# Kernel tuning notes

Hardware: AMD Instinct MI355X
Metric: run time of the kernel (lower is better)

## Reference

```python
import jax, jax.numpy as jnp
import numpy as np


def setup_inputs() -> dict:
    key = jax.random.key(0)
    k0, k1, k2, k3, k4, k5 = jax.random.split(key, 6)
    B, V, Fin, K, Fout = 8, 49152, 64, 3, 64
    nnz = V * 8  # ~8 neighbors per vertex (HEALPix sphere graph)
    std = (2.0 / (Fin * K)) ** 0.5  # Kaiming-normal as in reset_parameters
    inputs = jax.random.normal(k0, (B, V, Fin), jnp.float32)
    weight = jax.random.normal(k1, (Fin, K, Fout), jnp.float32) * std
    bias = jax.random.normal(k2, (Fout,), jnp.float32) * 0.05
    lap_rows = jax.random.randint(k3, (nnz,), 0, V, jnp.int32)
    lap_cols = jax.random.randint(k4, (nnz,), 0, V, jnp.int32)
    lap_vals = jax.random.normal(k5, (nnz,), jnp.float32) * 0.1
    return {"inputs": inputs, "weight": weight, "bias": bias,
            "lap_rows": lap_rows, "lap_cols": lap_cols, "lap_vals": lap_vals}


def reference(inputs, weight, bias, lap_rows, lap_cols, lap_vals):
    B, V, Fin = inputs.shape
    _, K, Fout = weight.shape

    def spmm(x):  # sparse Laplacian (COO) @ dense [V, Fin*B]
        return jax.ops.segment_sum(lap_vals[:, None] * x[lap_cols], lap_rows,
                                   num_segments=V)

    # x0: [V, Fin*B], matching torch's permute(1,2,0).view(V, Fin*B)
    x0 = inputs.transpose(1, 2, 0).reshape(V, Fin * B)
    xs = [x0]
    if K > 1:
        x1 = spmm(x0)
        xs.append(x1)
    for _ in range(2, K):
        x2 = 2.0 * spmm(x1) - x0  # Chebyshev recurrence
        xs.append(x2)
        x0, x1 = x1, x2
    x = jnp.stack(xs)                                    # [K, V, Fin*B]
    x = x.reshape(K, V, Fin, B).transpose(3, 1, 2, 0)    # [B, V, Fin, K]
    x = x.reshape(B * V, Fin * K)
    out = x @ weight.reshape(Fin * K, Fout)              # dense GEMM
    return out.reshape(B, V, Fout) + bias
```

## Files before the change

kernel.cpp:

```cpp
#include <hip/hip_runtime.h>
#include <hip/hip_bf16.h>
#include <stdint.h>

#define B_   8
#define V_   49152
#define M_   (B_ * V_)
#define GEMM_BLOCKS 1536

typedef unsigned short ushort_t;
typedef __attribute__((ext_vector_type(8))) short short8;
typedef __attribute__((ext_vector_type(4))) float float4v;

__device__ __forceinline__ float bf2f_lo(unsigned int pk) {
    union { unsigned int u; float f; } x; x.u = pk << 16; return x.f;
}
__device__ __forceinline__ float bf2f_hi(unsigned int pk) {
    union { unsigned int u; float f; } x; x.u = pk & 0xffff0000u; return x.f;
}
__device__ __forceinline__ ushort_t f2bf(float f) {
    union { unsigned int u; float f; } x; x.f = f;
    unsigned int u = x.u;
    unsigned int r = u + 0x7fffu + ((u >> 16) & 1u);
    return (ushort_t)(r >> 16);
}
__device__ __forceinline__ unsigned int pack2(float a, float b) {
    return ((unsigned int)f2bf(b) << 16) | (unsigned int)f2bf(a);
}

__global__ void fill_sentinel(float* out, int n) {
    int i = blockIdx.x * blockDim.x + threadIdx.x;
    if (i < n) out[i] = 9999.0f;
}

__global__ void zero_kernel(int* p, int n) {
    int i = blockIdx.x * blockDim.x + threadIdx.x;
    if (i < n) p[i] = 0;
}

__global__ void hist_kernel(const int* __restrict__ rows, int nnz, int* __restrict__ counts) {
    int i = blockIdx.x * blockDim.x + threadIdx.x;
    if (i < nnz) atomicAdd(&counts[rows[i]], 1);
}

__global__ __launch_bounds__(1024) void scan_kernel(const int* __restrict__ counts,
                                                    int* __restrict__ offsets) {
    __shared__ int s[1024];
    int t = threadIdx.x;
    const int C = V_ / 1024;
    int base_i = t * C;
    int sum = 0;
    for (int j = 0; j < C; j++) sum += counts[base_i + j];
    s[t] = sum;
    __syncthreads();
    for (int off = 1; off < 1024; off <<= 1) {
        int v = (t >= off) ? s[t - off] : 0;
        __syncthreads();
        s[t] += v;
        __syncthreads();
    }
    int run = (t == 0) ? 0 : s[t - 1];
    for (int j = 0; j < C; j++) {
        offsets[base_i + j] = run;
        run += counts[base_i + j];
    }
    if (t == 1023) offsets[V_] = run;
}

__global__ void bucket_kernel(const int* __restrict__ rows, const int* __restrict__ cols,
                              const float* __restrict__ vals, int nnz,
                              const int* __restrict__ offsets, int* __restrict__ cursor,
                              int* __restrict__ e_col, float* __restrict__ e_val) {
    int i = blockIdx.x * blockDim.x + threadIdx.x;
    if (i >= nnz) return;
    int r = rows[i];
    int p = offsets[r] + atomicAdd(&cursor[r], 1);
    e_col[p] = cols[i];
    e_val[p] = vals[i];
}

__global__ __launch_bounds__(256) void prep_x0t(const float* __restrict__ inp,
                                                ushort_t* __restrict__ x0t) {
    int idx = blockIdx.x * 256 + threadIdx.x;
    int f2 = idx & 31, v = idx >> 5;
    #pragma unroll
    for (int b = 0; b < 8; b++) {
        const float* src = inp + ((size_t)b * V_ + v) * 64 + f2 * 2;
        float2 d = *(const float2*)src;
        *(unsigned int*)(x0t + ((size_t)v * 8 + b) * 64 + f2 * 2) = pack2(d.x, d.y);
    }
}

__global__ void prep_w(const float* __restrict__ wgt, ushort_t* __restrict__ wBf) {
    int idx = blockIdx.x * 256 + threadIdx.x;
    if (idx >= 6 * 4 * 64 * 8) return;
    int j = idx & 7, lane = (idx >> 3) & 63, nt = (idx >> 9) & 3, kb = idx >> 11;
    int k = kb * 32 + (lane >> 4) * 8 + j;
    int kc = k >> 6, fi = k & 63;
    int fo = nt * 16 + (lane & 15);
    wBf[idx] = f2bf(wgt[(fi * 3 + kc) * 64 + fo]);
}

__global__ __launch_bounds__(256) void spmm1_kernel(const ushort_t* __restrict__ x0t,
                                                    const int* __restrict__ offsets,
                                                    const int* __restrict__ e_col,
                                                    const float* __restrict__ e_val,
                                                    ushort_t* __restrict__ x1) {
    int v = blockIdx.x, tid = threadIdx.x;
    int b = tid >> 5, f2 = tid & 31;
    int base = b * 64 + f2 * 2;
    __shared__ int   s_col[64];
    __shared__ float s_val[64];
    int beg = offsets[v], end = offsets[v + 1];
    float ax = 0.f, ay = 0.f;
    for (int c = beg; c < end; c += 64) {
        int n = min(64, end - c);
        if (tid < n) { s_col[tid] = e_col[c + tid]; s_val[tid] = e_val[c + tid]; }
        __syncthreads();
        for (int e = 0; e < n; e++) {
            unsigned int pk = *(const unsigned int*)(x0t + ((size_t)s_col[e] << 9) + base);
            float w = s_val[e];
            ax += w * bf2f_lo(pk);
            ay += w * bf2f_hi(pk);
        }
        __syncthreads();
    }
    *(unsigned int*)(x1 + ((size_t)v << 9) + base) = pack2(ax, ay);
}

__global__ __launch_bounds__(256) void spmm2_kernel(const ushort_t* __restrict__ x0t,
                                                    const ushort_t* __restrict__ x1,
                                                    const int* __restrict__ offsets,
                                                    const int* __restrict__ e_col,
                                                    const float* __restrict__ e_val,
                                                    ushort_t* __restrict__ x2) {
    int v = blockIdx.x, tid = threadIdx.x;
    int b = tid >> 5, f2 = tid & 31;
    int base = b * 64 + f2 * 2;
    __shared__ int   s_col[64];
    __shared__ float s_val[64];
    int beg = offsets[v], end = offsets[v + 1];
    float ax = 0.f, ay = 0.f;
    for (int c = beg; c < end; c += 64) {
        int n = min(64, end - c);
        if (tid < n) { s_col[tid] = e_col[c + tid]; s_val[tid] = e_val[c + tid]; }
        __syncthreads();
        for (int e = 0; e < n; e++) {
            unsigned int pk = *(const unsigned int*)(x1 + ((size_t)s_col[e] << 9) + base);
            float w = s_val[e];
            ax += w * bf2f_lo(pk);
            ay += w * bf2f_hi(pk);
        }
        __syncthreads();
    }
    unsigned int p0 = *(const unsigned int*)(x0t + ((size_t)v << 9) + base);
    float rx = 2.f * ax - bf2f_lo(p0);
    float ry = 2.f * ay - bf2f_hi(p0);
    *(unsigned int*)(x2 + ((size_t)v << 9) + base) = pack2(rx, ry);
}

__global__ __launch_bounds__(256) void gemm_kernel(const ushort_t* __restrict__ x0t,
                                                   const ushort_t* __restrict__ x1,
                                                   const ushort_t* __restrict__ x2,
                                                   const ushort_t* __restrict__ wBf,
                                                   const float* __restrict__ bias,
                                                   float* __restrict__ out) {
    int tid = threadIdx.x, lane = tid & 63, wv = tid >> 6;
    int quad = lane >> 4, col = lane & 15;

    short8 Bf[6][4];
    #pragma unroll
    for (int kb = 0; kb < 6; kb++)
        #pragma unroll
        for (int nt = 0; nt < 4; nt++)
            Bf[kb][nt] = *(const short8*)(wBf + ((size_t)((kb * 4 + nt) * 64 + lane)) * 8);

    float bv[4];
    #pragma unroll
    for (int nt = 0; nt < 4; nt++) bv[nt] = bias[nt * 16 + col];

    const int stride = GEMM_BLOCKS * 64;
    for (int m0 = (blockIdx.x * 4 + wv) * 16; m0 < M_; m0 += stride) {
        float4v acc[4];
        #pragma unroll
        for (int nt = 0; nt < 4; nt++) acc[nt] = (float4v){0.f, 0.f, 0.f, 0.f};

        const size_t arow = ((size_t)(m0 + col)) * 64 + quad * 8;
        #pragma unroll
        for (int kb = 0; kb < 6; kb++) {
            const ushort_t* src = (kb < 2) ? x0t : (kb < 4) ? x1 : x2;
            short8 A = *(const short8*)(src + arow + (kb & 1) * 32);
            #pragma unroll
            for (int nt = 0; nt < 4; nt++)
                acc[nt] = __builtin_amdgcn_mfma_f32_16x16x32_bf16(A, Bf[kb][nt], acc[nt], 0, 0, 0);
        }
        #pragma unroll
        for (int reg = 0; reg < 4; reg++) {
            int m = m0 + quad * 4 + reg;
            int v = m >> 3, b = m & 7;
            float* orow = out + ((size_t)b * V_ + v) * 64;
            #pragma unroll
            for (int nt = 0; nt < 4; nt++)
                orow[nt * 16 + col] = acc[nt][reg] + bv[nt];
        }
    }
}

extern "C" void kernel_launch(void* const* d_in, const int* in_sizes, int n_in,
                              void* d_out, int out_size, void* d_ws, size_t ws_size,
                              hipStream_t stream) {
    const float* inp  = (const float*)d_in[0];
    const float* wgt  = (const float*)d_in[1];
    const float* bias = (const float*)d_in[2];
    const int*   rows = (const int*)d_in[3];
    const int*   cols = (const int*)d_in[4];
    const float* vals = (const float*)d_in[5];
    int nnz = in_sizes[3];
    float* out = (float*)d_out;
    (void)n_in; (void)out_size;

    char* ws = (char*)d_ws;
    size_t o = 0;
    auto alloc = [&](size_t bytes) { void* p = ws + o; o += (bytes + 255) & ~(size_t)255; return p; };
    int*      counts  = (int*)alloc((size_t)V_ * 4);
    int*      cursor  = (int*)alloc((size_t)V_ * 4);
    int*      offsets = (int*)alloc(((size_t)V_ + 1) * 4);
    int*      e_col   = (int*)alloc((size_t)nnz * 4);
    float*    e_val   = (float*)alloc((size_t)nnz * 4);
    ushort_t* x0t     = (ushort_t*)alloc((size_t)M_ * 64 * 2);
    ushort_t* x1      = (ushort_t*)alloc((size_t)M_ * 64 * 2);
    ushort_t* x2      = (ushort_t*)alloc((size_t)M_ * 64 * 2);
    ushort_t* wBf     = (ushort_t*)alloc(6 * 4 * 64 * 8 * 2);

    if (ws_size < o) {
        fill_sentinel<<<(M_ * 64 + 255) / 256, 256, 0, stream>>>(out, M_ * 64);
        return;
    }

    zero_kernel<<<(2 * V_ + 255) / 256, 256, 0, stream>>>(counts, 2 * V_);
    hist_kernel<<<(nnz + 255) / 256, 256, 0, stream>>>(rows, nnz, counts);
    scan_kernel<<<1, 1024, 0, stream>>>(counts, offsets);
    bucket_kernel<<<(nnz + 255) / 256, 256, 0, stream>>>(rows, cols, vals, nnz,
                                                         offsets, cursor, e_col, e_val);
    prep_x0t<<<(V_ * 32) / 256, 256, 0, stream>>>(inp, x0t);
    prep_w<<<48, 256, 0, stream>>>(wgt, wBf);
    spmm1_kernel<<<V_, 256, 0, stream>>>(x0t, offsets, e_col, e_val, x1);
    spmm2_kernel<<<V_, 256, 0, stream>>>(x0t, x1, offsets, e_col, e_val, x2);
    gemm_kernel<<<GEMM_BLOCKS, 256, 0, stream>>>(x0t, x1, x2, wBf, bias, out);
}
```

Before: 428.9 us.

## Fuse second SpMM into GEMM and vectorize gathers with 8 vertices per block

Fuses the second Chebyshev SpMM step into the MFMA GEMM. The x2 tile is staged in LDS and consumed there, so x2 is never written to or read back from global memory. Both SpMM kernels now handle 8 vertices per block, with each thread gathering 32 bytes per neighbor and processing 4 edges per unrolled step. This replaces the old 256-thread-per-vertex layout that read 4 bytes per thread and staged edges through shared memory with syncs. The cost is higher register pressure from 16 accumulators plus the 24 weight fragments held in registers in the fused kernel, which may lower occupancy.

New measurement: 391.9 us. 1.09x faster.

```diff
diff --git a/kernel.cpp b/kernel.cpp
--- a/kernel.cpp
+++ b/kernel.cpp
@@ -1,11 +1,9 @@
 #include <hip/hip_runtime.h>
-#include <hip/hip_bf16.h>
 #include <stdint.h>
 
 #define B_   8
 #define V_   49152
 #define M_   (B_ * V_)
-#define GEMM_BLOCKS 1536
 
 typedef unsigned short ushort_t;
 typedef __attribute__((ext_vector_type(8))) short short8;
@@ -25,6 +23,14 @@
 }
 __device__ __forceinline__ unsigned int pack2(float a, float b) {
     return ((unsigned int)f2bf(b) << 16) | (unsigned int)f2bf(a);
+}
+__device__ __forceinline__ void fma8(float* acc, float w, const uint4& p) {
+    const unsigned int* u = (const unsigned int*)&p;
+    #pragma unroll
+    for (int i = 0; i < 4; i++) {
+        acc[2 * i]     += w * bf2f_lo(u[i]);
+        acc[2 * i + 1] += w * bf2f_hi(u[i]);
+    }
 }
 
 __global__ void fill_sentinel(float* out, int n) {
@@ -100,71 +106,95 @@
     wBf[idx] = f2bf(wgt[(fi * 3 + kc) * 64 + fo]);
 }
 
+__device__ __forceinline__ void gather16(const ushort_t* __restrict__ src,
+                                         const int* __restrict__ e_col,
+                                         const float* __restrict__ e_val,
+                                         int beg, int end, int b, int f8, float* acc) {
+    int e = beg;
+    for (; e + 4 <= end; e += 4) {
+        int c0 = e_col[e], c1 = e_col[e + 1], c2 = e_col[e + 2], c3 = e_col[e + 3];
+        float w0 = e_val[e], w1 = e_val[e + 1], w2 = e_val[e + 2], w3 = e_val[e + 3];
+        const ushort_t* p0 = src + ((size_t)c0 * 512) + b * 64 + f8 * 16;
+        const ushort_t* p1 = src + ((size_t)c1 * 512) + b * 64 + f8 * 16;
+        const ushort_t* p2 = src + ((size_t)c2 * 512) + b * 64 + f8 * 16;
+        const ushort_t* p3 = src + ((size_t)c3 * 512) + b * 64 + f8 * 16;
+        uint4 a0 = *(const uint4*)p0, b0 = *(const uint4*)(p0 + 8);
+        uint4 a1 = *(const uint4*)p1, b1 = *(const uint4*)(p1 + 8);
+        uint4 a2 = *(const uint4*)p2, b2 = *(const uint4*)(p2 + 8);
+        uint4 a3 = *(const uint4*)p3, b3 = *(const uint4*)(p3 + 8);
+        fma8(acc, w0, a0); fma8(acc + 8, w0, b0);
+        fma8(acc, w1, a1); fma8(acc + 8, w1, b1);
+        fma8(acc, w2, a2); fma8(acc + 8, w2, b2);
+        fma8(acc, w3, a3); fma8(acc + 8, w3, b3);
+    }
+    for (; e < end; e++) {
+        int c = e_col[e];
+        float w = e_val[e];
+        const ushort_t* p = src + ((size_t)c * 512) + b * 64 + f8 * 16;
+        uint4 a = *(const uint4*)p, bq = *(const uint4*)(p + 8);
+        fma8(acc, w, a); fma8(acc + 8, w, bq);
+    }
+}
+
 __global__ __launch_bounds__(256) void spmm1_kernel(const ushort_t* __restrict__ x0t,
                                                     const int* __restrict__ offsets,
                                                     const int* __restrict__ e_col,
                                                     const float* __restrict__ e_val,
                                                     ushort_t* __restrict__ x1) {
-    int v = blockIdx.x, tid = threadIdx.x;
-    int b = tid >> 5, f2 = tid & 31;
-    int base = b * 64 + f2 * 2;
-    __shared__ int   s_col[64];
-    __shared__ float s_val[64];
-    int beg = offsets[v], end = offsets[v + 1];
-    float ax = 0.f, ay = 0.f;
-    for (int c = beg; c < end; c += 64) {
-        int n = min(64, end - c);
-        if (tid < n) { s_col[tid] = e_col[c + tid]; s_val[tid] = e_val[c + tid]; }
-        __syncthreads();
-        for (int e = 0; e < n; e++) {
-            unsigned int pk = *(const unsigned int*)(x0t + ((size_t)s_col[e] << 9) + base);
-            float w = s_val[e];
-            ax += w * bf2f_lo(pk);
-            ay += w * bf2f_hi(pk);
-        }
-        __syncthreads();
-    }
-    *(unsigned int*)(x1 + ((size_t)v << 9) + base) = pack2(ax, ay);
-}
-
-__global__ __launch_bounds__(256) void spmm2_kernel(const ushort_t* __restrict__ x0t,
-                                                    const ushort_t* __restrict__ x1,
-                                                    const int* __restrict__ offsets,
-                                                    const int* __restrict__ e_col,
-                                                    const float* __restrict__ e_val,
-                                                    ushort_t* __restrict__ x2) {
-    int v = blockIdx.x, tid = threadIdx.x;
-    int b = tid >> 5, f2 = tid & 31;
-    int base = b * 64 + f2 * 2;
-    __shared__ int   s_col[64];
-    __shared__ float s_val[64];
-    int beg = offsets[v], end = offsets[v + 1];
-    float ax = 0.f, ay = 0.f;
-    for (int c = beg; c < end; c += 64) {
-        int n = min(64, end - c);
-        if (tid < n) { s_col[tid] = e_col[c + tid]; s_val[tid] = e_val[c + tid]; }
-        __syncthreads();
-        for (int e = 0; e < n; e++) {
-            unsigned int pk = *(const unsigned int*)(x1 + ((size_t)s_col[e] << 9) + base);
-            float w = s_val[e];
-            ax += w * bf2f_lo(pk);
-            ay += w * bf2f_hi(pk);
-        }
-        __syncthreads();
-    }
-    unsigned int p0 = *(const unsigned int*)(x0t + ((size_t)v << 9) + base);
-    float rx = 2.f * ax - bf2f_lo(p0);
-    float ry = 2.f * ay - bf2f_hi(p0);
-    *(unsigned int*)(x2 + ((size_t)v << 9) + base) = pack2(rx, ry);
-}
-
-__global__ __launch_bounds__(256) void gemm_kernel(const ushort_t* __restrict__ x0t,
-                                                   const ushort_t* __restrict__ x1,
-                                                   const ushort_t* __restrict__ x2,
-                                                   const ushort_t* __restrict__ wBf,
-                                                   const float* __restrict__ bias,
-                                                   float* __restrict__ out) {
-    int tid = threadIdx.x, lane = tid & 63, wv = tid >> 6;
+    int t = threadIdx.x;
+    int vi = t >> 5, b = (t >> 2) & 7, f8 = t & 3;
+    int v = blockIdx.x * 8 + vi;
+    float acc[16];
+    #pragma unroll
+    for (int i = 0; i < 16; i++) acc[i] = 0.f;
+    gather16(x0t, e_col, e_val, offsets[v], offsets[v + 1], b, f8, acc);
+    unsigned int opk[8];
+    #pragma unroll
+    for (int i = 0; i < 8; i++) opk[i] = pack2(acc[2 * i], acc[2 * i + 1]);
+    ushort_t* dst = x1 + ((size_t)v * 8 + b) * 64 + f8 * 16;
+    *(uint4*)dst       = make_uint4(opk[0], opk[1], opk[2], opk[3]);
+    *(uint4*)(dst + 8) = make_uint4(opk[4], opk[5], opk[6], opk[7]);
+}
+
+__global__ __launch_bounds__(256) void spmm2_gemm(const ushort_t* __restrict__ x0t,
+                                                  const ushort_t* __restrict__ x1,
+                                                  const int* __restrict__ offsets,
+                                                  const int* __restrict__ e_col,
+                                                  const float* __restrict__ e_val,
+                                                  const ushort_t* __restrict__ wBf,
+                                                  const float* __restrict__ bias,
+                                                  float* __restrict__ out) {
+    __shared__ ushort_t sh[64 * 72];
+    int t = threadIdx.x;
+    int vi = t >> 5, b = (t >> 2) & 7, f8 = t & 3;
+    int v0 = blockIdx.x * 8;
+    int v = v0 + vi;
+    float acc[16];
+    #pragma unroll
+    for (int i = 0; i < 16; i++) acc[i] = 0.f;
+    gather16(x1, e_col, e_val, offsets[v], offsets[v + 1], b, f8, acc);
+
+    size_t r = (size_t)v * 8 + b;
+    const ushort_t* x0p = x0t + r * 64 + f8 * 16;
+    uint4 qa = *(const uint4*)x0p, qb = *(const uint4*)(x0p + 8);
+    const unsigned int* ua = (const unsigned int*)&qa;
+    const unsigned int* ub = (const unsigned int*)&qb;
+    unsigned int opk[8];
+    #pragma unroll
+    for (int i = 0; i < 4; i++)
+        opk[i] = pack2(2.f * acc[2 * i] - bf2f_lo(ua[i]),
+                       2.f * acc[2 * i + 1] - bf2f_hi(ua[i]));
+    #pragma unroll
+    for (int i = 0; i < 4; i++)
+        opk[4 + i] = pack2(2.f * acc[8 + 2 * i] - bf2f_lo(ub[i]),
+                           2.f * acc[8 + 2 * i + 1] - bf2f_hi(ub[i]));
+    int mg = vi * 8 + b;
+    ushort_t* dst = sh + mg * 72 + f8 * 16;
+    *(uint4*)dst       = make_uint4(opk[0], opk[1], opk[2], opk[3]);
+    *(uint4*)(dst + 8) = make_uint4(opk[4], opk[5], opk[6], opk[7]);
+    __syncthreads();
+
+    int lane = t & 63, wv = t >> 6;
     int quad = lane >> 4, col = lane & 15;
 
     short8 Bf[6][4];
@@ -178,30 +208,42 @@
     #pragma unroll
     for (int nt = 0; nt < 4; nt++) bv[nt] = bias[nt * 16 + col];
 
-    const int stride = GEMM_BLOCKS * 64;
-    for (int m0 = (blockIdx.x * 4 + wv) * 16; m0 < M_; m0 += stride) {
-        float4v acc[4];
-        #pragma unroll
-        for (int nt = 0; nt < 4; nt++) acc[nt] = (float4v){0.f, 0.f, 0.f, 0.f};
-
-        const size_t arow = ((size_t)(m0 + col)) * 64 + quad * 8;
-        #pragma unroll
-        for (int kb = 0; kb < 6; kb++) {
-            const ushort_t* src = (kb < 2) ? x0t : (kb < 4) ? x1 : x2;
-            short8 A = *(const short8*)(src + arow + (kb & 1) * 32);
-            #pragma unroll
-            for (int nt = 0; nt < 4; nt++)
-                acc[nt] = __builtin_amdgcn_mfma_f32_16x16x32_bf16(A, Bf[kb][nt], acc[nt], 0, 0, 0);
-        }
-        #pragma unroll
-        for (int reg = 0; reg < 4; reg++) {
-            int m = m0 + quad * 4 + reg;
-            int v = m >> 3, b = m & 7;
-            float* orow = out + ((size_t)b * V_ + v) * 64;
-            #pragma unroll
-            for (int nt = 0; nt < 4; nt++)
-                orow[nt * 16 + col] = acc[nt][reg] + bv[nt];
-        }
+    float4v accm[4];
+    #pragma unroll
+    for (int nt = 0; nt < 4; nt++) accm[nt] = (float4v){0.f, 0.f, 0.f, 0.f};
+
+    int m0 = v0 * 8 + wv * 16;
+    size_t arow = (size_t)(m0 + col) * 64 + quad * 8;
+    #pragma unroll
+    for (int p = 0; p < 2; p++) {
+        short8 A = *(const short8*)(x0t + arow + p * 32);
+        #pragma unroll
+        for (int nt = 0; nt < 4; nt++)
+            accm[nt] = __builtin_amdgcn_mfma_f32_16x16x32_bf16(A, Bf[p][nt], accm[nt], 0, 0, 0);
+    }
+    #pragma unroll
+    for (int p = 0; p < 2; p++) {
+        short8 A = *(const short8*)(x1 + arow + p * 32);
+        #pragma unroll
+        for (int nt = 0; nt < 4; nt++)
+            accm[nt] = __builtin_amdgcn_mfma_f32_16x16x32_bf16(A, Bf[2 + p][nt], accm[nt], 0, 0, 0);
+    }
+    #pragma unroll
+    for (int p = 0; p < 2; p++) {
+        short8 A = *(const short8*)(sh + (wv * 16 + col) * 72 + quad * 8 + p * 32);
+        #pragma unroll
+        for (int nt = 0; nt < 4; nt++)
+            accm[nt] = __builtin_amdgcn_mfma_f32_16x16x32_bf16(A, Bf[4 + p][nt], accm[nt], 0, 0, 0);
+    }
+
+    #pragma unroll
+    for (int reg = 0; reg < 4; reg++) {
+        int m = m0 + quad * 4 + reg;
+        int vv = m >> 3, bb = m & 7;
+        float* orow = out + ((size_t)bb * V_ + vv) * 64;
+        #pragma unroll
+        for (int nt = 0; nt < 4; nt++)
+            orow[nt * 16 + col] = accm[nt][reg] + bv[nt];
     }
 }
 
@@ -228,7 +270,6 @@
     float*    e_val   = (float*)alloc((size_t)nnz * 4);
     ushort_t* x0t     = (ushort_t*)alloc((size_t)M_ * 64 * 2);
     ushort_t* x1      = (ushort_t*)alloc((size_t)M_ * 64 * 2);
-    ushort_t* x2      = (ushort_t*)alloc((size_t)M_ * 64 * 2);
     ushort_t* wBf     = (ushort_t*)alloc(6 * 4 * 64 * 8 * 2);
 
     if (ws_size < o) {
@@ -243,7 +284,6 @@
                                                          offsets, cursor, e_col, e_val);
     prep_x0t<<<(V_ * 32) / 256, 256, 0, stream>>>(inp, x0t);
     prep_w<<<48, 256, 0, stream>>>(wgt, wBf);
-    spmm1_kernel<<<V_, 256, 0, stream>>>(x0t, offsets, e_col, e_val, x1);
-    spmm2_kernel<<<V_, 256, 0, stream>>>(x0t, x1, offsets, e_col, e_val, x2);
-    gemm_kernel<<<GEMM_BLOCKS, 256, 0, stream>>>(x0t, x1, x2, wBf, bias, out);
-}
+    spmm1_kernel<<<V_ / 8, 256, 0, stream>>>(x0t, offsets, e_col, e_val, x1);
+    spmm2_gemm<<<V_ / 8, 256, 0, stream>>>(x0t, x1, offsets, e_col, e_val, wBf, bias, out);
+}
```
